# Optimization experiments

Hardware: AMD Instinct MI355X
Metric: run time of the kernel (lower is better)

## Reference

```python
import jax, jax.numpy as jnp
import numpy as np

SPACE_DIM = 3
D = SPACE_DIM + 1            # (t, x, y, z)
D_MODEL = 1024
N_LAYERS = 4                 # hidden layers
N_MIX = 64
TRI = D * (D - 1) // 2       # strict upper-triangular entries of A
OUT_DIM = N_MIX * (TRI + 1)  # per-mixture triu values + mixture logits
TRIU_I, TRIU_J = np.triu_indices(D, k=1)
RHO_SCALE = 10.0


def setup_inputs() -> dict:
    key = jax.random.key(0)
    ks = jax.random.split(key, 8)
    B = 65536
    x = jax.random.normal(ks[0], (B, D), jnp.float32)
    W0 = jax.random.normal(ks[1], (D, D_MODEL), jnp.float32) * np.float32(np.sqrt(2.0 / D))
    b0 = jnp.zeros((D_MODEL,), jnp.float32)
    Wh = jax.random.normal(ks[2], (N_LAYERS, D_MODEL, D_MODEL), jnp.float32) * np.float32(np.sqrt(2.0 / D_MODEL))
    bh = jnp.zeros((N_LAYERS, D_MODEL), jnp.float32)
    Wout = jax.random.normal(ks[3], (D_MODEL, OUT_DIM), jnp.float32) * np.float32(np.sqrt(1.0 / D_MODEL))
    bout = jnp.zeros((OUT_DIM,), jnp.float32)
    return dict(x=x, W0=W0, b0=b0, Wh=Wh, bh=bh, Wout=Wout, bout=bout)


def _mlp(z, W0, b0, Wh, bh, Wout, bout):
    # z: (D,) -> (OUT_DIM,), swish MLP (NeuralConservationLaw backbone)
    h = jax.nn.silu(z @ W0 + b0)
    for l in range(N_LAYERS):  # fixed small layer count: python loop ok
        h = jax.nn.silu(h @ Wh[l] + bh[l])
    return h @ Wout + bout


def _A(z, params):
    # Antisymmetric matrix field A(z): mixture-weighted strict-upper-tri values.
    out = _mlp(z, *params)                              # (OUT_DIM,)
    logits = out[:N_MIX]                                # (N_MIX,)
    vals = out[N_MIX:].reshape(N_MIX, TRI)              # (N_MIX, TRI)
    a = jax.nn.softmax(logits) @ vals                   # (TRI,)
    A = jnp.zeros((D, D), out.dtype).at[TRIU_I, TRIU_J].set(a)
    return A - A.T                                      # antisymmetric (D, D)


def reference(x, W0, b0, Wh, bh, Wout, bout):
    params = (W0, b0, Wh, bh, Wout, bout)

    def u_single(z):
        # u_i = sum_j dA_ij/dz_j  (row-divergence of antisymmetric A => div u = 0)
        J = jax.jacfwd(lambda zz: _A(zz, params))(z)    # (D, D, D): J[i,j,k]=dA_ij/dz_k
        return jnp.einsum('ijj->i', J)                  # (D,)

    u = jax.vmap(u_single)(x)                           # (B, D)
    rho = u[..., :1] * RHO_SCALE
    flux = u[..., 1:]
    return jnp.concatenate([rho, flux], axis=-1)
```

## Files before the change

kernel.cpp:

```cpp
#include <hip/hip_runtime.h>
#include <hip/hip_bf16.h>

typedef _Float16 half8 __attribute__((ext_vector_type(8)));
typedef _Float16 half4 __attribute__((ext_vector_type(4)));
typedef float floatx4 __attribute__((ext_vector_type(4)));

__device__ __forceinline__ float bfu2f(unsigned short u) {
  return __uint_as_float(((unsigned)u) << 16);
}

__device__ __forceinline__ void gld16(const void* g, void* l) {
  __builtin_amdgcn_global_load_lds((const __attribute__((address_space(1))) void*)g,
                                   (__attribute__((address_space(3))) void*)l, 16, 0, 0);
}

__device__ __forceinline__ float fast_sig(float v) {
  return __builtin_amdgcn_rcpf(1.f + __expf(-v));
}

template <int NC>
__device__ __forceinline__ void xcd_decode(int lin, int NR, int& r, int& c) {
  if (NR & 7) {
    c = lin % NC;
    r = lin / NC;
  } else {
    int rl = lin & 7;
    int t = lin >> 3;
    c = t % NC;
    r = (t / NC) * 8 + rl;
  }
}

__global__ void probe_kernel(const unsigned short* __restrict__ w0, int* __restrict__ flag) {
  __shared__ int s;
  if (threadIdx.x == 0) s = 0;
  __syncthreads();
  int big = 0;
  for (int i = threadIdx.x; i < 2048; i += 256) {
    unsigned e = (w0[i] >> 7) & 0xFFu;
    if (e >= 134u) big = 1;
  }
  if (big) atomicOr(&s, 1);
  __syncthreads();
  if (threadIdx.x == 0) *flag = s;
}

__global__ void cvt_kernel(const void* __restrict__ in, _Float16* __restrict__ out, int nOut,
                           int nIn, const int* __restrict__ flag) {
  int i = blockIdx.x * 256 + threadIdx.x;
  if (i >= nOut) return;
  float v = 0.f;
  if (i < nIn) v = (*flag) ? ((const float*)in)[i] : bfu2f(((const unsigned short*)in)[i]);
  out[i] = (_Float16)v;
}

__global__ void tr_kernel(const void* __restrict__ in, _Float16* __restrict__ out, int Nin,
                          long inStride, long outStride, const int* __restrict__ flag) {
  __shared__ float tile[32][33];
  const int f = *flag;
  int k0 = blockIdx.x * 32, n0 = blockIdx.y * 32;
  long ib = (long)blockIdx.z * inStride;
  long ob = (long)blockIdx.z * outStride;
  int tx = threadIdx.x, ty = threadIdx.y;
#pragma unroll
  for (int i = 0; i < 4; i++) {
    int k = k0 + ty + i * 8, n = n0 + tx;
    float v = 0.f;
    if (n < Nin) {
      long idx = ib + (long)k * Nin + n;
      v = f ? ((const float*)in)[idx] : bfu2f(((const unsigned short*)in)[idx]);
    }
    tile[ty + i * 8][tx] = v;
  }
  __syncthreads();
#pragma unroll
  for (int i = 0; i < 4; i++) {
    int n = n0 + ty + i * 8, k = k0 + tx;
    out[ob + (long)n * 1024 + k] = (_Float16)tile[tx][ty + i * 8];
  }
}

__global__ __launch_bounds__(256)
void layer0_kernel(const _Float16* __restrict__ x16, const _Float16* __restrict__ W0c,
                   const _Float16* __restrict__ b0c, _Float16* __restrict__ H,
                   int chunkBase, int S1) {
  const int lb = blockIdx.x;
  const int t = threadIdx.x;
  const long gb = (long)chunkBase + lb;
  float z0 = (float)x16[gb * 4 + 0];
  float z1 = (float)x16[gb * 4 + 1];
  float z2 = (float)x16[gb * 4 + 2];
  float z3 = (float)x16[gb * 4 + 3];
  const int j0 = t * 4;
  float w[4][4];
#pragma unroll
  for (int i = 0; i < 4; i++) {
    half4 wv = *(const half4*)&W0c[i * 1024 + j0];
#pragma unroll
    for (int jj = 0; jj < 4; jj++) w[i][jj] = (float)wv[jj];
  }
  half4 o[5];
#pragma unroll
  for (int jj = 0; jj < 4; jj++) {
    float pre = z0 * w[0][jj] + z1 * w[1][jj] + z2 * w[2][jj] + z3 * w[3][jj] +
                (float)b0c[j0 + jj];
    float s = fast_sig(pre);
    o[0][jj] = (_Float16)(pre * s);
    float ds = s * (1.f + pre * (1.f - s));
    o[1][jj] = (_Float16)(ds * w[0][jj]);
    o[2][jj] = (_Float16)(ds * w[1][jj]);
    o[3][jj] = (_Float16)(ds * w[2][jj]);
    o[4][jj] = (_Float16)(ds * w[3][jj]);
  }
  long rowbase = (long)lb * 1024 + j0;
#pragma unroll
  for (int s = 0; s < 5; s++) *(half4*)&H[(long)s * S1 + rowbase] = o[s];
}

__global__ __launch_bounds__(256, 3)
void gemm_h1(const _Float16* __restrict__ A, const _Float16* __restrict__ Bt,
             const _Float16* __restrict__ bias, _Float16* __restrict__ C,
             _Float16* __restrict__ DS, int NR) {
  constexpr int K = 1024;
  __shared__ _Float16 SM[8192];
  _Float16* As = SM;
  _Float16* Bs = SM + 4096;
  _Float16* Ep = SM;
  const int tid = threadIdx.x;
  const int wave = tid >> 6;
  const int lane = tid & 63;
  int rb, cb;
  xcd_decode<8>(blockIdx.x, NR, rb, cb);
  const int n0 = cb * 128;
  const long m0 = (long)rb * 128;

  const int srow0 = (wave * 2 + 0) * 16 + (lane >> 2);
  const int srow1 = (wave * 2 + 1) * 16 + (lane >> 2);
  const int scol = (lane & 3) * 8;
  const _Float16* gA0 = A + (m0 + srow0) * K + scol;
  const _Float16* gA1 = A + (m0 + srow1) * K + scol;
  const _Float16* gB0 = Bt + (long)(n0 + srow0) * K + scol;
  const _Float16* gB1 = Bt + (long)(n0 + srow1) * K + scol;
  _Float16* lA0 = As + (wave * 2 + 0) * 512;
  _Float16* lA1 = As + (wave * 2 + 1) * 512;
  _Float16* lB0 = Bs + (wave * 2 + 0) * 512;
  _Float16* lB1 = Bs + (wave * 2 + 1) * 512;

  const int wm = (wave & 1) * 64;
  const int wn = (wave >> 1) * 64;
  const int fr = lane & 15;
  const int fc = (lane >> 4) * 8;
  const int c0f = lane & 15;
  const int rqk = lane >> 4;
  const int myRound = wave & 1;

  float bv[4];
#pragma unroll
  for (int ni = 0; ni < 4; ni++) bv[ni] = (float)bias[n0 + wn + ni * 16 + c0f];

  const int erow = tid >> 4;
  const int ecol = (tid & 15) * 8;
  const int ecolp = ecol ^ (wave << 4);

  floatx4 acc[4][4];
#pragma unroll
  for (int i = 0; i < 4; i++)
#pragma unroll
    for (int j = 0; j < 4; j++) acc[i][j] = (floatx4)(0.f);

  for (int kk = 0; kk < K; kk += 32) {
    __syncthreads();
    gld16(gA0 + kk, lA0);
    gld16(gA1 + kk, lA1);
    gld16(gB0 + kk, lB0);
    gld16(gB1 + kk, lB1);
    __syncthreads();
    half8 af[4], bf[4];
#pragma unroll
    for (int i = 0; i < 4; i++) af[i] = *(const half8*)&As[(wm + i * 16 + fr) * 32 + fc];
#pragma unroll
    for (int i = 0; i < 4; i++) bf[i] = *(const half8*)&Bs[(wn + i * 16 + fr) * 32 + fc];
#pragma unroll
    for (int mi = 0; mi < 4; mi++)
#pragma unroll
      for (int ni = 0; ni < 4; ni++)
        acc[mi][ni] = __builtin_amdgcn_mfma_f32_16x16x32_f16(af[mi], bf[ni], acc[mi][ni], 0, 0, 0);
  }

#pragma unroll
  for (int r = 0; r < 2; r++) {
    __syncthreads();
    if (myRound == r) {
#pragma unroll
      for (int mi = 0; mi < 4; mi++)
#pragma unroll
        for (int ni = 0; ni < 4; ni++) {
          int colp = (wn + ni * 16 + c0f) ^ (rqk << 4);
#pragma unroll
          for (int rr = 0; rr < 4; rr++) {
            int row_local = mi * 16 + rqk * 4 + rr;
            Ep[row_local * 128 + colp] = (_Float16)(acc[mi][ni][rr] + bv[ni]);
          }
        }
    }
    __syncthreads();
#pragma unroll
    for (int p = 0; p < 4; p++) {
      int row_local = p * 16 + erow;
      half8 vv = *(const half8*)&Ep[row_local * 128 + ecolp];
      long row = m0 + r * 64 + row_local;
      half8 hv, dv;
#pragma unroll
      for (int e = 0; e < 8; e++) {
        float xv = (float)vv[e];
        float sg = fast_sig(xv);
        hv[e] = (_Float16)(xv * sg);
        dv[e] = (_Float16)(sg * (1.f + xv * (1.f - sg)));
      }
      *(half8*)&C[row * (long)K + n0 + ecol] = hv;
      *(half8*)&DS[row * (long)K + n0 + ecol] = dv;
    }
  }
}

__global__ __launch_bounds__(256, 4)
void gemm_h2(const _Float16* __restrict__ A, const _Float16* __restrict__ Bt,
             _Float16* __restrict__ C, const _Float16* __restrict__ DS, int bcMask, int NR) {
  constexpr int K = 1024;
  __shared__ _Float16 SM[8192];
  _Float16* As = SM;
  _Float16* Bs = SM + 4096;
  _Float16* Ep = SM;
  const int tid = threadIdx.x;
  const int wave = tid >> 6;
  const int lane = tid & 63;
  int rb, cb;
  xcd_decode<8>(blockIdx.x, NR, rb, cb);
  const int n0 = cb * 128;
  const long m0 = (long)rb * 128;

  const int srow0 = (wave * 2 + 0) * 16 + (lane >> 2);
  const int srow1 = (wave * 2 + 1) * 16 + (lane >> 2);
  const int scol = (lane & 3) * 8;
  const _Float16* gA0 = A + (m0 + srow0) * K + scol;
  const _Float16* gA1 = A + (m0 + srow1) * K + scol;
  const _Float16* gB0 = Bt + (long)(n0 + srow0) * K + scol;
  const _Float16* gB1 = Bt + (long)(n0 + srow1) * K + scol;
  _Float16* lA0 = As + (wave * 2 + 0) * 512;
  _Float16* lA1 = As + (wave * 2 + 1) * 512;
  _Float16* lB0 = Bs + (wave * 2 + 0) * 512;
  _Float16* lB1 = Bs + (wave * 2 + 1) * 512;

  const int wm = (wave & 1) * 64;
  const int wn = (wave >> 1) * 64;
  const int fr = lane & 15;
  const int fc = (lane >> 4) * 8;
  const int c0f = lane & 15;
  const int rqk = lane >> 4;
  const int myRound = wave & 1;

  const int erow = tid >> 4;
  const int ecol = (tid & 15) * 8;
  const int ecolp = ecol ^ (wave << 4);

  floatx4 acc[4][4];
#pragma unroll
  for (int i = 0; i < 4; i++)
#pragma unroll
    for (int j = 0; j < 4; j++) acc[i][j] = (floatx4)(0.f);

  for (int kk = 0; kk < K; kk += 32) {
    __syncthreads();
    gld16(gA0 + kk, lA0);
    gld16(gA1 + kk, lA1);
    gld16(gB0 + kk, lB0);
    gld16(gB1 + kk, lB1);
    __syncthreads();
    half8 af[4], bf[4];
#pragma unroll
    for (int i = 0; i < 4; i++) af[i] = *(const half8*)&As[(wm + i * 16 + fr) * 32 + fc];
#pragma unroll
    for (int i = 0; i < 4; i++) bf[i] = *(const half8*)&Bs[(wn + i * 16 + fr) * 32 + fc];
#pragma unroll
    for (int mi = 0; mi < 4; mi++)
#pragma unroll
      for (int ni = 0; ni < 4; ni++)
        acc[mi][ni] = __builtin_amdgcn_mfma_f32_16x16x32_f16(af[mi], bf[ni], acc[mi][ni], 0, 0, 0);
  }

#pragma unroll
  for (int r = 0; r < 2; r++) {
    __syncthreads();
    if (myRound == r) {
#pragma unroll
      for (int mi = 0; mi < 4; mi++)
#pragma unroll
        for (int ni = 0; ni < 4; ni++) {
          int colp = (wn + ni * 16 + c0f) ^ (rqk << 4);
#pragma unroll
          for (int rr = 0; rr < 4; rr++) {
            int row_local = mi * 16 + rqk * 4 + rr;
            Ep[row_local * 128 + colp] = (_Float16)acc[mi][ni][rr];
          }
        }
    }
    __syncthreads();
#pragma unroll
    for (int p = 0; p < 4; p++) {
      int row_local = p * 16 + erow;
      half8 vv = *(const half8*)&Ep[row_local * 128 + ecolp];
      long row = m0 + r * 64 + row_local;
      half8 dv = *(const half8*)&DS[(long)(row & bcMask) * K + n0 + ecol];
      *(half8*)&C[row * (long)K + n0 + ecol] = dv * vv;
    }
  }
}

__global__ __launch_bounds__(256, 4)
void gemm_out(const _Float16* __restrict__ A, const _Float16* __restrict__ Bt,
              const _Float16* __restrict__ bias, _Float16* __restrict__ C,
              int Nreal, int ldc, int biasRows, int NR) {
  constexpr int K = 1024;
  __shared__ _Float16 SM[8192];
  _Float16* As = SM;
  _Float16* Bs = SM + 4096;
  _Float16* Ep = SM;
  const int tid = threadIdx.x;
  const int wave = tid >> 6;
  const int lane = tid & 63;
  int rb, cb;
  xcd_decode<4>(blockIdx.x, NR, rb, cb);
  const int n0 = cb * 128;
  const long m0 = (long)rb * 128;

  const int srow0 = (wave * 2 + 0) * 16 + (lane >> 2);
  const int srow1 = (wave * 2 + 1) * 16 + (lane >> 2);
  const int scol = (lane & 3) * 8;
  const _Float16* gA0 = A + (m0 + srow0) * K + scol;
  const _Float16* gA1 = A + (m0 + srow1) * K + scol;
  const _Float16* gB0 = Bt + (long)(n0 + srow0) * K + scol;
  const _Float16* gB1 = Bt + (long)(n0 + srow1) * K + scol;
  _Float16* lA0 = As + (wave * 2 + 0) * 512;
  _Float16* lA1 = As + (wave * 2 + 1) * 512;
  _Float16* lB0 = Bs + (wave * 2 + 0) * 512;
  _Float16* lB1 = Bs + (wave * 2 + 1) * 512;

  const int wm = (wave & 1) * 64;
  const int wn = (wave >> 1) * 64;
  const int fr = lane & 15;
  const int fc = (lane >> 4) * 8;
  const int c0f = lane & 15;
  const int rqk = lane >> 4;
  const int myRound = wave & 1;

  float bv[4];
#pragma unroll
  for (int ni = 0; ni < 4; ni++) bv[ni] = (float)bias[n0 + wn + ni * 16 + c0f];

  const int erow = tid >> 4;
  const int ecol = (tid & 15) * 8;
  const int ecolp = ecol ^ (wave << 4);

  floatx4 acc[4][4];
#pragma unroll
  for (int i = 0; i < 4; i++)
#pragma unroll
    for (int j = 0; j < 4; j++) acc[i][j] = (floatx4)(0.f);

  for (int kk = 0; kk < K; kk += 32) {
    __syncthreads();
    gld16(gA0 + kk, lA0);
    gld16(gA1 + kk, lA1);
    gld16(gB0 + kk, lB0);
    gld16(gB1 + kk, lB1);
    __syncthreads();
    half8 af[4], bf[4];
#pragma unroll
    for (int i = 0; i < 4; i++) af[i] = *(const half8*)&As[(wm + i * 16 + fr) * 32 + fc];
#pragma unroll
    for (int i = 0; i < 4; i++) bf[i] = *(const half8*)&Bs[(wn + i * 16 + fr) * 32 + fc];
#pragma unroll
    for (int mi = 0; mi < 4; mi++)
#pragma unroll
      for (int ni = 0; ni < 4; ni++)
        acc[mi][ni] = __builtin_amdgcn_mfma_f32_16x16x32_f16(af[mi], bf[ni], acc[mi][ni], 0, 0, 0);
  }

#pragma unroll
  for (int r = 0; r < 2; r++) {
    __syncthreads();
    if (myRound == r) {
#pragma unroll
      for (int mi = 0; mi < 4; mi++)
#pragma unroll
        for (int ni = 0; ni < 4; ni++) {
          int colp = (wn + ni * 16 + c0f) ^ (rqk << 4);
#pragma unroll
          for (int rr = 0; rr < 4; rr++) {
            int row_local = mi * 16 + rqk * 4 + rr;
            long grow = m0 + wm + mi * 16 + rqk * 4 + rr;
            float v = acc[mi][ni][rr] + (grow < biasRows ? bv[ni] : 0.f);
            Ep[row_local * 128 + colp] = (_Float16)v;
          }
        }
    }
    __syncthreads();
#pragma unroll
    for (int p = 0; p < 4; p++) {
      int row_local = p * 16 + erow;
      int col = n0 + ecol;
      if (col < Nreal) {
        half8 vv = *(const half8*)&Ep[row_local * 128 + ecolp];
        long row = m0 + r * 64 + row_local;
        *(half8*)&C[row * (long)ldc + col] = vv;
      }
    }
  }
}

__global__ __launch_bounds__(256)
void finalize_kernel(const _Float16* __restrict__ O5, void* __restrict__ outp,
                     int chunkBase, int Bc, const int* __restrict__ flag) {
  const int wid = threadIdx.x >> 6;
  const int lane = threadIdx.x & 63;
  const int lb = blockIdx.x * 4 + wid;
  const long SO = (long)Bc * 448;
  const long base0 = (long)lb * 448;

  union UU { unsigned u; _Float16 h[2]; };

  float lg = (float)O5[base0 + lane];
  float vals[6];
  {
    const unsigned* vp = (const unsigned*)(O5 + base0 + 64 + lane * 6);
#pragma unroll
    for (int q = 0; q < 3; q++) {
      UU c; c.u = vp[q];
      vals[2 * q] = (float)c.h[0];
      vals[2 * q + 1] = (float)c.h[1];
    }
  }
  float dl[4], dv[4][6];
#pragma unroll
  for (int t = 0; t < 4; t++) {
    long bs = (long)(1 + t) * SO + base0;
    dl[t] = (float)O5[bs + lane];
    const unsigned* vp = (const unsigned*)(O5 + bs + 64 + lane * 6);
#pragma unroll
    for (int q = 0; q < 3; q++) {
      UU c; c.u = vp[q];
      dv[t][2 * q] = (float)c.h[0];
      dv[t][2 * q + 1] = (float)c.h[1];
    }
  }
  float mx = lg;
#pragma unroll
  for (int off = 32; off >= 1; off >>= 1) mx = fmaxf(mx, __shfl_xor(mx, off));
  float e = __expf(lg - mx);
  float S = e;
#pragma unroll
  for (int off = 32; off >= 1; off >>= 1) S += __shfl_xor(S, off);
  float pv = e / S;
  float st[4];
#pragma unroll
  for (int t = 0; t < 4; t++) {
    float v = pv * dl[t];
#pragma unroll
    for (int off = 32; off >= 1; off >>= 1) v += __shfl_xor(v, off);
    st[t] = v;
  }
  float da[4][6];
#pragma unroll
  for (int t = 0; t < 4; t++) {
    float w = pv * (dl[t] - st[t]);
#pragma unroll
    for (int k = 0; k < 6; k++) {
      float v = w * vals[k] + pv * dv[t][k];
#pragma unroll
      for (int off = 32; off >= 1; off >>= 1) v += __shfl_xor(v, off);
      da[t][k] = v;
    }
  }
  if (lane == 0) {
    float u0 = da[1][0] + da[2][1] + da[3][2];
    float u1 = -da[0][0] + da[2][3] + da[3][4];
    float u2 = -da[0][1] - da[1][3] + da[3][5];
    float u3 = -da[0][2] - da[1][4] - da[2][5];
    long ob = (long)(chunkBase + lb) * 4;
    if (*flag) {
      float* o = (float*)outp;
      o[ob] = 10.f * u0; o[ob + 1] = u1; o[ob + 2] = u2; o[ob + 3] = u3;
    } else {
      __hip_bfloat16* o = (__hip_bfloat16*)outp;
      o[ob] = __float2bfloat16(10.f * u0);
      o[ob + 1] = __float2bfloat16(u1);
      o[ob + 2] = __float2bfloat16(u2);
      o[ob + 3] = __float2bfloat16(u3);
    }
  }
}

extern "C" void kernel_launch(void* const* d_in, const int* in_sizes, int n_in,
                              void* d_out, int out_size, void* d_ws, size_t ws_size,
                              hipStream_t stream) {
  const void* x = d_in[0];
  const void* W0 = d_in[1];
  const void* b0 = d_in[2];
  const void* Wh = d_in[3];
  const void* bh = d_in[4];
  const void* Wout = d_in[5];
  const void* bout = d_in[6];
  const int B = in_sizes[0] / 4;

  char* p = (char*)d_ws;
  int* flag = (int*)p;                 p += 256;
  _Float16* W0c = (_Float16*)p;        p += 4096 * 2;
  _Float16* b0c = (_Float16*)p;        p += 1024 * 2;
  _Float16* bhc = (_Float16*)p;        p += 4096 * 2;
  _Float16* boutc = (_Float16*)p;      p += 512 * 2;
  p += 256 - ((size_t)(p - (char*)d_ws) & 255);
  _Float16* x16 = (_Float16*)p;        p += (size_t)B * 4 * 2;
  _Float16* WhT = (_Float16*)p;        p += (size_t)4 * 1024 * 1024 * 2;
  _Float16* WoutT = (_Float16*)p;      p += (size_t)512 * 1024 * 2;
  size_t used = (size_t)(p - (char*)d_ws);
  size_t rem = (ws_size > used) ? (ws_size - used) : 0;
  const size_t perS = 10240 + 10240 + 2048 + 4480;
  long bcap = (long)(rem / perS);
  int Bc = 128;
  while ((long)Bc * 2 <= bcap && Bc * 2 <= B) Bc *= 2;
  _Float16* Ha = (_Float16*)p;         p += (size_t)5 * Bc * 1024 * 2;
  _Float16* Hb = (_Float16*)p;         p += (size_t)5 * Bc * 1024 * 2;
  _Float16* DS = (_Float16*)p;         p += (size_t)Bc * 1024 * 2;
  _Float16* PREo = (_Float16*)p;

  probe_kernel<<<1, 256, 0, stream>>>((const unsigned short*)W0, flag);
  cvt_kernel<<<(B * 4 + 255) / 256, 256, 0, stream>>>(x, x16, B * 4, B * 4, flag);
  cvt_kernel<<<16, 256, 0, stream>>>(W0, W0c, 4096, 4096, flag);
  cvt_kernel<<<4, 256, 0, stream>>>(b0, b0c, 1024, 1024, flag);
  cvt_kernel<<<16, 256, 0, stream>>>(bh, bhc, 4096, 4096, flag);
  cvt_kernel<<<2, 256, 0, stream>>>(bout, boutc, 512, 448, flag);
  tr_kernel<<<dim3(32, 32, 4), dim3(32, 8), 0, stream>>>(Wh, WhT, 1024, 1024L * 1024, 1024L * 1024, flag);
  tr_kernel<<<dim3(32, 16, 1), dim3(32, 8), 0, stream>>>(Wout, WoutT, 448, 0L, 0L, flag);

  const int nChunks = B / Bc;
  for (int c = 0; c < nChunks; c++) {
    const int base = c * Bc;
    const int S1 = Bc * 1024;
    _Float16* Hin = Ha;
    _Float16* Hout = Hb;
    layer0_kernel<<<Bc, 256, 0, stream>>>(x16, W0c, b0c, Hin, base, S1);
    const int NR1 = Bc / 128;
    const int NR2 = 4 * Bc / 128;
    const int NRo = 5 * Bc / 128;
    for (int l = 0; l < 4; l++) {
      const _Float16* Wl = WhT + (size_t)l * 1024 * 1024;
      gemm_h1<<<8 * NR1, 256, 0, stream>>>(
          Hin, Wl, bhc + l * 1024, Hout, DS, NR1);
      gemm_h2<<<8 * NR2, 256, 0, stream>>>(
          Hin + S1, Wl, Hout + S1, DS, Bc - 1, NR2);
      _Float16* t = Hin; Hin = Hout; Hout = t;
    }
    gemm_out<<<4 * NRo, 256, 0, stream>>>(
        Hin, WoutT, boutc, PREo, 448, 448, Bc, NRo);
    finalize_kernel<<<Bc / 4, 256, 0, stream>>>(PREo, d_out, base, Bc, flag);
  }
}
```

Before: 4.666 ms.

## Load GEMM fragments directly from global into registers with register double-buffering

Removes the LDS staging and the two barriers per k-step in gemm_h2. Each wave now loads its MFMA A/B fragments straight from global memory into registers and prefetches the next k-step while the current MFMAs run. Occupancy hint drops from 4 to 3 blocks per SU to make room for the extra registers. This gives up data sharing across waves (each A/B row is fetched by two waves) and uses narrow 16-byte strided global loads that depend on L1/L2 hit rates.

```diff
diff --git a/kernel.cpp b/kernel.cpp
--- a/kernel.cpp
+++ b/kernel.cpp
@@ -223,14 +223,11 @@
   }
 }
 
-__global__ __launch_bounds__(256, 4)
+__global__ __launch_bounds__(256, 3)
 void gemm_h2(const _Float16* __restrict__ A, const _Float16* __restrict__ Bt,
              _Float16* __restrict__ C, const _Float16* __restrict__ DS, int bcMask, int NR) {
   constexpr int K = 1024;
-  __shared__ _Float16 SM[8192];
-  _Float16* As = SM;
-  _Float16* Bs = SM + 4096;
-  _Float16* Ep = SM;
+  __shared__ _Float16 Ep[8192];
   const int tid = threadIdx.x;
   const int wave = tid >> 6;
   const int lane = tid & 63;
@@ -239,18 +236,6 @@
   const int n0 = cb * 128;
   const long m0 = (long)rb * 128;
 
-  const int srow0 = (wave * 2 + 0) * 16 + (lane >> 2);
-  const int srow1 = (wave * 2 + 1) * 16 + (lane >> 2);
-  const int scol = (lane & 3) * 8;
-  const _Float16* gA0 = A + (m0 + srow0) * K + scol;
-  const _Float16* gA1 = A + (m0 + srow1) * K + scol;
-  const _Float16* gB0 = Bt + (long)(n0 + srow0) * K + scol;
-  const _Float16* gB1 = Bt + (long)(n0 + srow1) * K + scol;
-  _Float16* lA0 = As + (wave * 2 + 0) * 512;
-  _Float16* lA1 = As + (wave * 2 + 1) * 512;
-  _Float16* lB0 = Bs + (wave * 2 + 0) * 512;
-  _Float16* lB1 = Bs + (wave * 2 + 1) * 512;
-
   const int wm = (wave & 1) * 64;
   const int wn = (wave >> 1) * 64;
   const int fr = lane & 15;
@@ -259,6 +244,14 @@
   const int rqk = lane >> 4;
   const int myRound = wave & 1;
 
+  const _Float16* baseA[4];
+  const _Float16* baseB[4];
+#pragma unroll
+  for (int i = 0; i < 4; i++) {
+    baseA[i] = A + (m0 + wm + i * 16 + fr) * (long)K + fc;
+    baseB[i] = Bt + (long)(n0 + wn + i * 16 + fr) * K + fc;
+  }
+
   const int erow = tid >> 4;
   const int ecol = (tid & 15) * 8;
   const int ecolp = ecol ^ (wave << 4);
@@ -269,23 +262,30 @@
 #pragma unroll
     for (int j = 0; j < 4; j++) acc[i][j] = (floatx4)(0.f);
 
-  for (int kk = 0; kk < K; kk += 32) {
-    __syncthreads();
-    gld16(gA0 + kk, lA0);
-    gld16(gA1 + kk, lA1);
-    gld16(gB0 + kk, lB0);
-    gld16(gB1 + kk, lB1);
-    __syncthreads();
-    half8 af[4], bf[4];
-#pragma unroll
-    for (int i = 0; i < 4; i++) af[i] = *(const half8*)&As[(wm + i * 16 + fr) * 32 + fc];
-#pragma unroll
-    for (int i = 0; i < 4; i++) bf[i] = *(const half8*)&Bs[(wn + i * 16 + fr) * 32 + fc];
+  half8 a0[4], b0[4], a1[4], b1[4];
+#pragma unroll
+  for (int i = 0; i < 4; i++) a0[i] = *(const half8*)(baseA[i]);
+#pragma unroll
+  for (int i = 0; i < 4; i++) b0[i] = *(const half8*)(baseB[i]);
+
+#pragma unroll
+  for (int it = 0; it < 32; ++it) {
+    if (it < 31) {
+      const int kk = (it + 1) * 32;
+#pragma unroll
+      for (int i = 0; i < 4; i++) a1[i] = *(const half8*)(baseA[i] + kk);
+#pragma unroll
+      for (int i = 0; i < 4; i++) b1[i] = *(const half8*)(baseB[i] + kk);
+    }
 #pragma unroll
     for (int mi = 0; mi < 4; mi++)
 #pragma unroll
       for (int ni = 0; ni < 4; ni++)
-        acc[mi][ni] = __builtin_amdgcn_mfma_f32_16x16x32_f16(af[mi], bf[ni], acc[mi][ni], 0, 0, 0);
+        acc[mi][ni] = __builtin_amdgcn_mfma_f32_16x16x32_f16(a0[mi], b0[ni], acc[mi][ni], 0, 0, 0);
+    if (it < 31) {
+#pragma unroll
+      for (int i = 0; i < 4; i++) { a0[i] = a1[i]; b0[i] = b1[i]; }
+    }
   }
 
 #pragma unroll
```

Measured after the change: 9.925 ms. 113% more time.

## Register-prefetch next K tile and pad LDS rows in the three GEMM kernels

Applied to the files above, without the earlier changes.

Direct global-to-LDS loads are replaced with register staging in the three GEMM kernels. Each thread now loads the next 32-wide K slice into registers while the MFMAs run on the current slice, then writes it to LDS at the top of the next iteration. LDS rows are padded from 32 to 40 halves to reduce bank conflicts on fragment reads. The cost is more LDS per block and more registers, and launch bounds drop from 4 to 3 blocks per CU for two kernels.

```diff
diff --git a/kernel.cpp b/kernel.cpp
--- a/kernel.cpp
+++ b/kernel.cpp
@@ -7,11 +7,6 @@
 
 __device__ __forceinline__ float bfu2f(unsigned short u) {
   return __uint_as_float(((unsigned)u) << 16);
-}
-
-__device__ __forceinline__ void gld16(const void* g, void* l) {
-  __builtin_amdgcn_global_load_lds((const __attribute__((address_space(1))) void*)g,
-                                   (__attribute__((address_space(3))) void*)l, 16, 0, 0);
 }
 
 __device__ __forceinline__ float fast_sig(float v) {
@@ -30,6 +25,9 @@
     r = (t / NC) * 8 + rl;
   }
 }
+
+#define LDA 40
+#define BOFF 5120
 
 __global__ void probe_kernel(const unsigned short* __restrict__ w0, int* __restrict__ flag) {
   __shared__ int s;
@@ -122,9 +120,7 @@
              const _Float16* __restrict__ bias, _Float16* __restrict__ C,
              _Float16* __restrict__ DS, int NR) {
   constexpr int K = 1024;
-  __shared__ _Float16 SM[8192];
-  _Float16* As = SM;
-  _Float16* Bs = SM + 4096;
+  __shared__ _Float16 SM[10240];
   _Float16* Ep = SM;
   const int tid = threadIdx.x;
   const int wave = tid >> 6;
@@ -141,10 +137,10 @@
   const _Float16* gA1 = A + (m0 + srow1) * K + scol;
   const _Float16* gB0 = Bt + (long)(n0 + srow0) * K + scol;
   const _Float16* gB1 = Bt + (long)(n0 + srow1) * K + scol;
-  _Float16* lA0 = As + (wave * 2 + 0) * 512;
-  _Float16* lA1 = As + (wave * 2 + 1) * 512;
-  _Float16* lB0 = Bs + (wave * 2 + 0) * 512;
-  _Float16* lB1 = Bs + (wave * 2 + 1) * 512;
+  _Float16* wA0 = SM + srow0 * LDA + scol;
+  _Float16* wA1 = SM + srow1 * LDA + scol;
+  _Float16* wB0 = SM + BOFF + srow0 * LDA + scol;
+  _Float16* wB1 = SM + BOFF + srow1 * LDA + scol;
 
   const int wm = (wave & 1) * 64;
   const int wn = (wave >> 1) * 64;
@@ -168,18 +164,30 @@
 #pragma unroll
     for (int j = 0; j < 4; j++) acc[i][j] = (floatx4)(0.f);
 
-  for (int kk = 0; kk < K; kk += 32) {
-    __syncthreads();
-    gld16(gA0 + kk, lA0);
-    gld16(gA1 + kk, lA1);
-    gld16(gB0 + kk, lB0);
-    gld16(gB1 + kk, lB1);
-    __syncthreads();
+  half8 ra0 = *(const half8*)gA0;
+  half8 ra1 = *(const half8*)gA1;
+  half8 rb0 = *(const half8*)gB0;
+  half8 rb1 = *(const half8*)gB1;
+
+  for (int it = 0; it < 32; ++it) {
+    __syncthreads();
+    *(half8*)wA0 = ra0;
+    *(half8*)wA1 = ra1;
+    *(half8*)wB0 = rb0;
+    *(half8*)wB1 = rb1;
+    __syncthreads();
+    if (it < 31) {
+      const int kk = (it + 1) * 32;
+      ra0 = *(const half8*)(gA0 + kk);
+      ra1 = *(const half8*)(gA1 + kk);
+      rb0 = *(const half8*)(gB0 + kk);
+      rb1 = *(const half8*)(gB1 + kk);
+    }
     half8 af[4], bf[4];
 #pragma unroll
-    for (int i = 0; i < 4; i++) af[i] = *(const half8*)&As[(wm + i * 16 + fr) * 32 + fc];
-#pragma unroll
-    for (int i = 0; i < 4; i++) bf[i] = *(const half8*)&Bs[(wn + i * 16 + fr) * 32 + fc];
+    for (int i = 0; i < 4; i++) af[i] = *(const half8*)&SM[(wm + i * 16 + fr) * LDA + fc];
+#pragma unroll
+    for (int i = 0; i < 4; i++) bf[i] = *(const half8*)&SM[BOFF + (wn + i * 16 + fr) * LDA + fc];
 #pragma unroll
     for (int mi = 0; mi < 4; mi++)
 #pragma unroll
@@ -223,13 +231,11 @@
   }
 }
 
-__global__ __launch_bounds__(256, 4)
+__global__ __launch_bounds__(256, 3)
 void gemm_h2(const _Float16* __restrict__ A, const _Float16* __restrict__ Bt,
              _Float16* __restrict__ C, const _Float16* __restrict__ DS, int bcMask, int NR) {
   constexpr int K = 1024;
-  __shared__ _Float16 SM[8192];
-  _Float16* As = SM;
-  _Float16* Bs = SM + 4096;
+  __shared__ _Float16 SM[10240];
   _Float16* Ep = SM;
   const int tid = threadIdx.x;
   const int wave = tid >> 6;
@@ -246,10 +252,10 @@
   const _Float16* gA1 = A + (m0 + srow1) * K + scol;
   const _Float16* gB0 = Bt + (long)(n0 + srow0) * K + scol;
   const _Float16* gB1 = Bt + (long)(n0 + srow1) * K + scol;
-  _Float16* lA0 = As + (wave * 2 + 0) * 512;
-  _Float16* lA1 = As + (wave * 2 + 1) * 512;
-  _Float16* lB0 = Bs + (wave * 2 + 0) * 512;
-  _Float16* lB1 = Bs + (wave * 2 + 1) * 512;
+  _Float16* wA0 = SM + srow0 * LDA + scol;
+  _Float16* wA1 = SM + srow1 * LDA + scol;
+  _Float16* wB0 = SM + BOFF + srow0 * LDA + scol;
+  _Float16* wB1 = SM + BOFF + srow1 * LDA + scol;
 
   const int wm = (wave & 1) * 64;
   const int wn = (wave >> 1) * 64;
@@ -269,18 +275,30 @@
 #pragma unroll
     for (int j = 0; j < 4; j++) acc[i][j] = (floatx4)(0.f);
 
-  for (int kk = 0; kk < K; kk += 32) {
-    __syncthreads();
-    gld16(gA0 + kk, lA0);
-    gld16(gA1 + kk, lA1);
-    gld16(gB0 + kk, lB0);
-    gld16(gB1 + kk, lB1);
-    __syncthreads();
+  half8 ra0 = *(const half8*)gA0;
+  half8 ra1 = *(const half8*)gA1;
+  half8 rb0 = *(const half8*)gB0;
+  half8 rb1 = *(const half8*)gB1;
+
+  for (int it = 0; it < 32; ++it) {
+    __syncthreads();
+    *(half8*)wA0 = ra0;
+    *(half8*)wA1 = ra1;
+    *(half8*)wB0 = rb0;
+    *(half8*)wB1 = rb1;
+    __syncthreads();
+    if (it < 31) {
+      const int kk = (it + 1) * 32;
+      ra0 = *(const half8*)(gA0 + kk);
+      ra1 = *(const half8*)(gA1 + kk);
+      rb0 = *(const half8*)(gB0 + kk);
+      rb1 = *(const half8*)(gB1 + kk);
+    }
     half8 af[4], bf[4];
 #pragma unroll
-    for (int i = 0; i < 4; i++) af[i] = *(const half8*)&As[(wm + i * 16 + fr) * 32 + fc];
-#pragma unroll
-    for (int i = 0; i < 4; i++) bf[i] = *(const half8*)&Bs[(wn + i * 16 + fr) * 32 + fc];
+    for (int i = 0; i < 4; i++) af[i] = *(const half8*)&SM[(wm + i * 16 + fr) * LDA + fc];
+#pragma unroll
+    for (int i = 0; i < 4; i++) bf[i] = *(const half8*)&SM[BOFF + (wn + i * 16 + fr) * LDA + fc];
 #pragma unroll
     for (int mi = 0; mi < 4; mi++)
 #pragma unroll
@@ -316,14 +334,12 @@
   }
 }
 
-__global__ __launch_bounds__(256, 4)
+__global__ __launch_bounds__(256, 3)
 void gemm_out(const _Float16* __restrict__ A, const _Float16* __restrict__ Bt,
               const _Float16* __restrict__ bias, _Float16* __restrict__ C,
               int Nreal, int ldc, int biasRows, int NR) {
   constexpr int K = 1024;
-  __shared__ _Float16 SM[8192];
-  _Float16* As = SM;
-  _Float16* Bs = SM + 4096;
+  __shared__ _Float16 SM[10240];
   _Float16* Ep = SM;
   const int tid = threadIdx.x;
   const int wave = tid >> 6;
@@ -340,10 +356,10 @@
   const _Float16* gA1 = A + (m0 + srow1) * K + scol;
   const _Float16* gB0 = Bt + (long)(n0 + srow0) * K + scol;
   const _Float16* gB1 = Bt + (long)(n0 + srow1) * K + scol;
-  _Float16* lA0 = As + (wave * 2 + 0) * 512;
-  _Float16* lA1 = As + (wave * 2 + 1) * 512;
-  _Float16* lB0 = Bs + (wave * 2 + 0) * 512;
-  _Float16* lB1 = Bs + (wave * 2 + 1) * 512;
+  _Float16* wA0 = SM + srow0 * LDA + scol;
+  _Float16* wA1 = SM + srow1 * LDA + scol;
+  _Float16* wB0 = SM + BOFF + srow0 * LDA + scol;
+  _Float16* wB1 = SM + BOFF + srow1 * LDA + scol;
 
   const int wm = (wave & 1) * 64;
   const int wn = (wave >> 1) * 64;
@@ -367,18 +383,30 @@
 #pragma unroll
     for (int j = 0; j < 4; j++) acc[i][j] = (floatx4)(0.f);
 
-  for (int kk = 0; kk < K; kk += 32) {
-    __syncthreads();
-    gld16(gA0 + kk, lA0);
-    gld16(gA1 + kk, lA1);
-    gld16(gB0 + kk, lB0);
-    gld16(gB1 + kk, lB1);
-    __syncthreads();
+  half8 ra0 = *(const half8*)gA0;
+  half8 ra1 = *(const half8*)gA1;
+  half8 rb0 = *(const half8*)gB0;
+  half8 rb1 = *(const half8*)gB1;
+
+  for (int it = 0; it < 32; ++it) {
+    __syncthreads();
+    *(half8*)wA0 = ra0;
+    *(half8*)wA1 = ra1;
+    *(half8*)wB0 = rb0;
+    *(half8*)wB1 = rb1;
+    __syncthreads();
+    if (it < 31) {
+      const int kk = (it + 1) * 32;
+      ra0 = *(const half8*)(gA0 + kk);
+      ra1 = *(const half8*)(gA1 + kk);
+      rb0 = *(const half8*)(gB0 + kk);
+      rb1 = *(const half8*)(gB1 + kk);
+    }
     half8 af[4], bf[4];
 #pragma unroll
-    for (int i = 0; i < 4; i++) af[i] = *(const half8*)&As[(wm + i * 16 + fr) * 32 + fc];
-#pragma unroll
-    for (int i = 0; i < 4; i++) bf[i] = *(const half8*)&Bs[(wn + i * 16 + fr) * 32 + fc];
+    for (int i = 0; i < 4; i++) af[i] = *(const half8*)&SM[(wm + i * 16 + fr) * LDA + fc];
+#pragma unroll
+    for (int i = 0; i < 4; i++) bf[i] = *(const half8*)&SM[BOFF + (wn + i * 16 + fr) * LDA + fc];
 #pragma unroll
     for (int mi = 0; mi < 4; mi++)
 #pragma unroll
```

Result: slower. 4.774 ms (+2.3%).
